# Kernel tuning notes

Measured on AMD Instinct MI355X. Metric: run time of the kernel, lower is better.

Reference implementation:

```python
import jax, jax.numpy as jnp
import numpy as np

HIDDEN = 1024
HEADS = 16
HEAD_DIM = HIDDEN // HEADS  # 64
B, S = 2, 2048


def setup_inputs() -> dict:
    key = jax.random.key(0)
    ks = jax.random.split(key, 12)
    lim_h = 1.0 / np.sqrt(HEAD_DIM)
    lim_o = 1.0 / np.sqrt(HIDDEN)
    u = lambda k, shape, lim: jax.random.uniform(k, shape, jnp.float32, -lim, lim)
    return {
        "query": jax.random.normal(ks[0], (B, S, HIDDEN), jnp.float32),
        "key": jax.random.normal(ks[1], (B, S, HIDDEN), jnp.float32),
        "value": jax.random.normal(ks[2], (B, S, HIDDEN), jnp.float32),
        "mask": jax.random.randint(ks[3], (B, 1, S, S), 0, 2, jnp.int32),
        "Wq": u(ks[4], (HEAD_DIM, HEAD_DIM), lim_h), "bq": u(ks[5], (HEAD_DIM,), lim_h),
        "Wk": u(ks[6], (HEAD_DIM, HEAD_DIM), lim_h), "bk": u(ks[7], (HEAD_DIM,), lim_h),
        "Wv": u(ks[8], (HEAD_DIM, HEAD_DIM), lim_h), "bv": u(ks[9], (HEAD_DIM,), lim_h),
        "Wo": u(ks[10], (HIDDEN, HIDDEN), lim_o), "bo": u(ks[11], (HIDDEN,), lim_o),
    }


def reference(query, key, value, mask, Wq, bq, Wk, bk, Wv, bv, Wo, bo):
    b = query.shape[0]
    # view [B, S, H, D]; per-head linear is SHARED across heads (head_dim x head_dim)
    q = query.reshape(b, -1, HEADS, HEAD_DIM) @ Wq.T + bq
    k = key.reshape(b, -1, HEADS, HEAD_DIM) @ Wk.T + bk
    v = value.reshape(b, -1, HEADS, HEAD_DIM) @ Wv.T + bv
    scores = jnp.einsum('nqhd,nkhd->nhqk', q, k)  # [B, H, Sq, Sk]
    scores = jnp.where(mask == 0, jnp.float32(-1e20), scores)
    # NOTE: original scales by sqrt(hidden_dim), not sqrt(head_dim)
    attn = jax.nn.softmax(scores / np.sqrt(HIDDEN).astype(np.float32), axis=3)
    out = jnp.einsum('nhql,nlhd->nqhd', attn, v).reshape(b, query.shape[1], HIDDEN)
    return out @ Wo.T + bo
```

## Files before the change

kernel.cpp:

```cpp
#include <hip/hip_runtime.h>
#include <hip/hip_bf16.h>

#define NB 2
#define NS 2048
#define NH 16
#define ND 64
#define NHID 1024

#define QSCALE 0.045084220f

typedef __attribute__((ext_vector_type(8))) short bf16x8;
typedef __attribute__((ext_vector_type(4))) short s16x4;
typedef __attribute__((ext_vector_type(4))) float f32x4;

typedef __attribute__((address_space(3))) unsigned int lds_u32;
typedef __attribute__((address_space(1))) unsigned int glb_u32;

__device__ inline void gl_lds16(const void* g, void* l) {
  __builtin_amdgcn_global_load_lds((const glb_u32*)g, (lds_u32*)l, 16, 0, 0);
}

__device__ inline short f2bf(float f) {
  __hip_bfloat16 h = __float2bfloat16(f);
  short s; __builtin_memcpy(&s, &h, 2); return s;
}

__device__ inline float selbit(float e, unsigned long long m) {
  float r;
  asm("v_cndmask_b32 %0, 0, %1, %2" : "=v"(r) : "v"(e), "s"(m));
  return r;
}

__device__ inline bf16x8 cvt8(const float* __restrict__ p) {
  float4 x = *(const float4*)p;
  float4 y = *(const float4*)(p + 4);
  bf16x8 r;
  r[0] = f2bf(x.x); r[1] = f2bf(x.y); r[2] = f2bf(x.z); r[3] = f2bf(x.w);
  r[4] = f2bf(y.x); r[5] = f2bf(y.y); r[6] = f2bf(y.z); r[7] = f2bf(y.w);
  return r;
}

__global__ __launch_bounds__(256) void prep(
    const int* __restrict__ mask, unsigned long long* __restrict__ mp,
    const float* __restrict__ Wq, const float* __restrict__ Wk,
    const float* __restrict__ Wv, const float* __restrict__ Wo,
    short* __restrict__ Wq_b, short* __restrict__ Wk_b,
    short* __restrict__ Wv_b, short* __restrict__ Wo_b)
{
  if (blockIdx.x < 512) {
    int tg = blockIdx.x * 256 + threadIdx.x;
    int q4 = tg & 3;
    int g4 = tg >> 2;
    int mt = g4 & 3, kt = (g4 >> 2) & 31, qg = (g4 >> 7) & 127, b = g4 >> 14;
    unsigned long long wq[4] = {0ull, 0ull, 0ull, 0ull};
#pragma unroll
    for (int cc = 0; cc < 4; ++cc) {
      int c2 = q4 * 4 + cc;
      const int4* p = (const int4*)(mask +
          ((size_t)(b * NS + qg * 16 + c2) * NS) + kt * 64 + mt * 16);
#pragma unroll
      for (int qq2 = 0; qq2 < 4; ++qq2) {
        int4 v = p[qq2];
        int sh = qq2 * 16 + c2;
        wq[0] |= (unsigned long long)(v.x != 0) << sh;
        wq[1] |= (unsigned long long)(v.y != 0) << sh;
        wq[2] |= (unsigned long long)(v.z != 0) << sh;
        wq[3] |= (unsigned long long)(v.w != 0) << sh;
      }
    }
#pragma unroll
    for (int r = 0; r < 4; ++r) {
      wq[r] |= __shfl_xor(wq[r], 1);
      wq[r] |= __shfl_xor(wq[r], 2);
    }
    mp[(size_t)g4 * 4 + q4] = wq[q4];
  } else {
    int i = ((blockIdx.x - 512) * 256 + threadIdx.x) * 4;
    const float* src; short* dst; int off; float sc = 1.0f;
    if (i < 1048576)      { src = Wo; dst = Wo_b; off = i; }
    else {
      int j = i - 1048576;
      if (j < 4096)       { src = Wq; dst = Wq_b; off = j; sc = QSCALE; }
      else if (j < 8192)  { src = Wk; dst = Wk_b; off = j - 4096; }
      else                { src = Wv; dst = Wv_b; off = j - 8192; }
    }
    float4 v = *(const float4*)(src + off);
    s16x4 o;
    o[0] = f2bf(v.x * sc); o[1] = f2bf(v.y * sc);
    o[2] = f2bf(v.z * sc); o[3] = f2bf(v.w * sc);
    *(s16x4*)(dst + off) = o;
  }
}

__global__ __launch_bounds__(256) void qk_proj(
    const float* __restrict__ qin, const float* __restrict__ kin,
    const short* __restrict__ Wq_b, const float* __restrict__ bq,
    const short* __restrict__ Wk_b, const float* __restrict__ bk,
    short* __restrict__ Qws, short* __restrict__ Kws)
{
  __shared__ __align__(16) short ldsT[4][16][72];
  const int tid = threadIdx.x;
  const int w = tid >> 6, lane = tid & 63;
  const int c = lane & 15, qq = lane >> 4;
  const int t = blockIdx.x * 4 + w;
  const int b = t >> 11, s = t & (NS - 1);
  const int aoff = (t * 16 + c) * 64 + qq * 8;
  const int row0 = lane >> 3, inner = lane & 7;

#pragma unroll
  for (int m = 0; m < 2; ++m) {
    const float* X  = (m == 0) ? qin  : kin;
    const short* W  = (m == 0) ? Wq_b : Wk_b;
    const float* bb = (m == 0) ? bq   : bk;
    short* dst      = (m == 0) ? Qws  : Kws;
    const float bsc = (m == 0) ? QSCALE : 1.0f;

    bf16x8 a0 = cvt8(X + aoff);
    bf16x8 a1 = cvt8(X + aoff + 32);

#pragma unroll
    for (int nt = 0; nt < 4; ++nt) {
      f32x4 z = {0.f, 0.f, 0.f, 0.f};
      const short* wp = W + (nt * 16 + c) * 64 + qq * 8;
      bf16x8 b0 = *(const bf16x8*)(wp);
      bf16x8 b1 = *(const bf16x8*)(wp + 32);
      z = __builtin_amdgcn_mfma_f32_16x16x32_bf16(a0, b0, z, 0, 0, 0);
      z = __builtin_amdgcn_mfma_f32_16x16x32_bf16(a1, b1, z, 0, 0, 0);
      float bias = bb[nt * 16 + c] * bsc;
#pragma unroll
      for (int r = 0; r < 4; ++r)
        ldsT[w][qq * 4 + r][nt * 16 + c] = f2bf(z[r] + bias);
    }

    bf16x8 v0 = *(const bf16x8*)&ldsT[w][row0][inner * 8];
    bf16x8 v1 = *(const bf16x8*)&ldsT[w][row0 + 8][inner * 8];
    int bh0 = b * NH + row0, bh1 = b * NH + row0 + 8;
    *(bf16x8*)(dst + (bh0 * NS + s) * 64 + inner * 8) = v0;
    *(bf16x8*)(dst + (bh1 * NS + s) * 64 + inner * 8) = v1;
  }
}

__global__ __launch_bounds__(256) void vproj(
    const float* __restrict__ vin, const short* __restrict__ Wv_b,
    const float* __restrict__ bv, short* __restrict__ Vt)
{
  __shared__ __align__(16) short ldsVT[64][72];
  const int tid = threadIdx.x;
  const int g = tid >> 6, lane = tid & 63;
  const int c = lane & 15, qq = lane >> 4;
  const int bh = blockIdx.x >> 5;
  const int stile = blockIdx.x & 31;
  const int b = bh >> 4, h = bh & 15;
  const int sb = stile * 64;

  bf16x8 wv[8];
  float bias[4];
#pragma unroll
  for (int nt = 0; nt < 4; ++nt) {
    const short* wp = Wv_b + (nt * 16 + c) * 64 + qq * 8;
    wv[nt * 2]     = *(const bf16x8*)(wp);
    wv[nt * 2 + 1] = *(const bf16x8*)(wp + 32);
    bias[nt] = bv[nt * 16 + c];
  }

  const float* ap = vin + ((size_t)((b * NS + sb + 16 * g + c) * 16 + h)) * 64 + qq * 8;
  bf16x8 a0 = cvt8(ap);
  bf16x8 a1 = cvt8(ap + 32);
#pragma unroll
  for (int nt = 0; nt < 4; ++nt) {
    f32x4 z = {0.f, 0.f, 0.f, 0.f};
    z = __builtin_amdgcn_mfma_f32_16x16x32_bf16(a0, wv[nt * 2], z, 0, 0, 0);
    z = __builtin_amdgcn_mfma_f32_16x16x32_bf16(a1, wv[nt * 2 + 1], z, 0, 0, 0);
    ushort4 u;
    u.x = (unsigned short)f2bf(z[0] + bias[nt]);
    u.y = (unsigned short)f2bf(z[1] + bias[nt]);
    u.z = (unsigned short)f2bf(z[2] + bias[nt]);
    u.w = (unsigned short)f2bf(z[3] + bias[nt]);
    *(ushort4*)&ldsVT[nt * 16 + c][16 * g + qq * 4] = u;
  }
  __syncthreads();

#pragma unroll
  for (int j = 0; j < 2; ++j) {
    int idx = tid + 256 * j;
    int d = idx >> 3, unit = idx & 7;
    bf16x8 o = *(const bf16x8*)&ldsVT[d][unit * 8];
    *(bf16x8*)(Vt + ((size_t)(bh * 64 + d)) * NS + sb + unit * 8) = o;
  }
}

__global__ __launch_bounds__(256, 4) void attn(
    const short* __restrict__ Qws, const short* __restrict__ Kws,
    const short* __restrict__ Vt, const unsigned long long* __restrict__ Mp,
    short* __restrict__ AO)
{
  __shared__ __align__(16) short Ks[2][64][64];
  __shared__ __align__(16) short Vs[2][64][64];
  __shared__ __align__(16) short Ps[4][16][64];

  const int tid = threadIdx.x;
  const int w = tid >> 6, lane = tid & 63;
  const int c = lane & 15, qq = lane >> 4;
  const int bh = blockIdx.x & 31;
  const int qtile = blockIdx.x >> 5;
  const int b = bh >> 4, h = bh & 15;
  const int qbase = qtile * 64 + w * 16;
  const int ca2 = (lane & 7) << 1;

  const short* Qp = Qws + (size_t)bh * (NS * 64);
  const short* Kp = Kws + (size_t)bh * (NS * 64);
  const short* Vp = Vt + (size_t)bh * (64 * NS);

  const int wu = __builtin_amdgcn_readfirstlane(w);
  const unsigned long long* mbase =
      Mp + (size_t)(b * (NS / 16) + qtile * 4 + wu) * ((NS / 64) * 16);

  bf16x8 aq0, aq1;
  {
    const short* qp = Qp + (qbase + c) * 64 + qq * 8;
    aq0 = *(const bf16x8*)(qp);
    aq1 = *(const bf16x8*)(qp + 32);
  }

  float lsum = 0.f;
  f32x4 O[4];
#pragma unroll
  for (int dt = 0; dt < 4; ++dt) { f32x4 z = {0.f, 0.f, 0.f, 0.f}; O[dt] = z; }

  short* Pw = &Ps[w][c][0];

  const int srow = lane >> 3;
  const int sunit = (lane & 7) ^ srow;
  auto stage = [&](int kt, int buf) {
#pragma unroll
    for (int i = 0; i < 2; ++i) {
      int j = w * 2 + i;
      const short* gk = Kp + ((size_t)(kt * 64 + j * 8 + srow)) * 64 + sunit * 8;
      gl_lds16(gk, &Ks[buf][0][0] + j * 512);
      const short* gv = Vp + ((size_t)(j * 8 + srow)) * NS + kt * 64 + sunit * 8;
      gl_lds16(gv, &Vs[buf][0][0] + j * 512);
    }
  };

  stage(0, 0);
  __syncthreads();

  for (int kt = 0; kt < NS / 64; ++kt) {
    const int buf = kt & 1;
    if (kt < NS / 64 - 1) stage(kt + 1, buf ^ 1);

    unsigned long long mw[16];
#pragma unroll
    for (int i = 0; i < 16; ++i) mw[i] = mbase[(size_t)kt * 16 + i];

    f32x4 st[4];
#pragma unroll
    for (int mt = 0; mt < 4; ++mt) {
      const short* kb = &Ks[buf][mt * 16 + c][0];
      bf16x8 ak0 = *(const bf16x8*)(kb + ((qq ^ (c & 7)) << 3));
      bf16x8 ak1 = *(const bf16x8*)(kb + (((4 + qq) ^ (c & 7)) << 3));
      f32x4 z = {0.f, 0.f, 0.f, 0.f};
      z = __builtin_amdgcn_mfma_f32_16x16x32_bf16(ak0, aq0, z, 0, 0, 0);
      z = __builtin_amdgcn_mfma_f32_16x16x32_bf16(ak1, aq1, z, 0, 0, 0);
      st[mt] = z;
    }

#pragma unroll
    for (int mt = 0; mt < 4; ++mt) {
      f32x4 s = st[mt];
      float e0 = selbit(__builtin_amdgcn_exp2f(s[0]), mw[mt * 4 + 0]);
      float e1 = selbit(__builtin_amdgcn_exp2f(s[1]), mw[mt * 4 + 1]);
      float e2 = selbit(__builtin_amdgcn_exp2f(s[2]), mw[mt * 4 + 2]);
      float e3 = selbit(__builtin_amdgcn_exp2f(s[3]), mw[mt * 4 + 3]);
      lsum += (e0 + e1) + (e2 + e3);
      ushort4 u;
      u.x = (unsigned short)f2bf(e0);
      u.y = (unsigned short)f2bf(e1);
      u.z = (unsigned short)f2bf(e2);
      u.w = (unsigned short)f2bf(e3);
      *(ushort4*)&Pw[((mt * 4 + qq) ^ ca2) << 2] = u;
    }

#pragma unroll
    for (int ks = 0; ks < 2; ++ks) {
      bf16x8 pf = *(const bf16x8*)&Pw[((ks * 8 + qq * 2) ^ ca2) << 2];
#pragma unroll
      for (int dt = 0; dt < 4; ++dt) {
        const short* vb = &Vs[buf][dt * 16 + c][0];
        bf16x8 vf = *(const bf16x8*)(vb + ((((ks << 2) + qq) ^ (c & 7)) << 3));
        O[dt] = __builtin_amdgcn_mfma_f32_16x16x32_bf16(vf, pf, O[dt], 0, 0, 0);
      }
    }

    __syncthreads();
  }

  {
    float v = lsum;
    v += __shfl_xor(v, 16);
    v += __shfl_xor(v, 32);
    lsum = 1.0f / fmaxf(v, 1e-30f);
  }

  const int row = qbase + c;
#pragma unroll
  for (int dt = 0; dt < 4; ++dt) {
    ushort4 u;
    u.x = (unsigned short)f2bf(O[dt][0] * lsum);
    u.y = (unsigned short)f2bf(O[dt][1] * lsum);
    u.z = (unsigned short)f2bf(O[dt][2] * lsum);
    u.w = (unsigned short)f2bf(O[dt][3] * lsum);
    *(ushort4*)(AO + ((size_t)(b * NS + row)) * NHID + h * 64 + dt * 16 + qq * 4) = u;
  }
}

__global__ __launch_bounds__(256, 2) void oproj(
    const short* __restrict__ X, const short* __restrict__ Wo_b,
    const float* __restrict__ bo, float* __restrict__ out)
{
  __shared__ __align__(16) short As[2][64][64];
  __shared__ __align__(16) short Bs[2][128][64];
  const int tid = threadIdx.x;
  const int w = tid >> 6, lane = tid & 63;
  const int c = lane & 15, qq = lane >> 4;
  const int rowbase = blockIdx.x * 64;
  const int colbase = blockIdx.y * 128;
  const int mh = w & 1, nh = w >> 1;

  const int srow = lane >> 3;
  const int sunit = (lane & 7) ^ srow;

  auto stage = [&](int kb, int buf) {
#pragma unroll
    for (int i = 0; i < 6; ++i) {
      int t = w * 6 + i;
      if (t < 8) {
        const short* g = X + (size_t)(rowbase + t * 8 + srow) * NHID
                           + kb * 64 + sunit * 8;
        gl_lds16(g, &As[buf][0][0] + t * 512);
      } else {
        int j = t - 8;
        const short* g = Wo_b + (size_t)(colbase + j * 8 + srow) * NHID
                              + kb * 64 + sunit * 8;
        gl_lds16(g, &Bs[buf][0][0] + j * 512);
      }
    }
  };

  f32x4 acc[2][4];
#pragma unroll
  for (int mt = 0; mt < 2; ++mt)
#pragma unroll
    for (int nt = 0; nt < 4; ++nt) { f32x4 z = {0.f, 0.f, 0.f, 0.f}; acc[mt][nt] = z; }

  stage(0, 0);
  __syncthreads();

  for (int kb = 0; kb < NHID / 64; ++kb) {
    const int buf = kb & 1;
    if (kb < NHID / 64 - 1) stage(kb + 1, buf ^ 1);

    bf16x8 af[2][2];
#pragma unroll
    for (int mt = 0; mt < 2; ++mt) {
      const short* ap = &As[buf][mh * 32 + mt * 16 + c][0];
#pragma unroll
      for (int ks = 0; ks < 2; ++ks)
        af[mt][ks] = *(const bf16x8*)(ap + ((((ks << 2) + qq) ^ (c & 7)) << 3));
    }
#pragma unroll
    for (int nt = 0; nt < 4; ++nt) {
      const short* bp = &Bs[buf][nh * 64 + nt * 16 + c][0];
#pragma unroll
      for (int ks = 0; ks < 2; ++ks) {
        bf16x8 bf = *(const bf16x8*)(bp + ((((ks << 2) + qq) ^ (c & 7)) << 3));
#pragma unroll
        for (int mt = 0; mt < 2; ++mt)
          acc[mt][nt] = __builtin_amdgcn_mfma_f32_16x16x32_bf16(af[mt][ks], bf, acc[mt][nt], 0, 0, 0);
      }
    }

    __syncthreads();
  }

#pragma unroll
  for (int nt = 0; nt < 4; ++nt) {
    int col = colbase + nh * 64 + nt * 16 + c;
    float bias = bo[col];
#pragma unroll
    for (int mt = 0; mt < 2; ++mt) {
      int row = rowbase + mh * 32 + mt * 16 + qq * 4;
#pragma unroll
      for (int r = 0; r < 4; ++r)
        out[(size_t)(row + r) * NHID + col] = acc[mt][nt][r] + bias;
    }
  }
}

extern "C" void kernel_launch(void* const* d_in, const int* in_sizes, int n_in,
                              void* d_out, int out_size, void* d_ws, size_t ws_size,
                              hipStream_t stream) {
  const float* qin = (const float*)d_in[0];
  const float* kin = (const float*)d_in[1];
  const float* vin = (const float*)d_in[2];
  const int*  mask = (const int*)d_in[3];
  const float* Wq = (const float*)d_in[4];
  const float* bq = (const float*)d_in[5];
  const float* Wk = (const float*)d_in[6];
  const float* bk = (const float*)d_in[7];
  const float* Wv = (const float*)d_in[8];
  const float* bv = (const float*)d_in[9];
  const float* Wo = (const float*)d_in[10];
  const float* bo = (const float*)d_in[11];
  float* out = (float*)d_out;

  char* ws = (char*)d_ws;
  short* Qws = (short*)(ws);
  short* Kws = (short*)(ws + (size_t)(8 << 20));
  short* Vt  = (short*)(ws + (size_t)(16 << 20));
  short* AO  = (short*)(ws + (size_t)(24 << 20));
  unsigned long long* Mp = (unsigned long long*)(ws + (size_t)(32 << 20));
  short* Wo_b = (short*)(ws + (size_t)(33 << 20));
  short* Wq_b = (short*)(ws + (size_t)(35 << 20));
  short* Wk_b = (short*)(ws + (size_t)(35 << 20) + 8192);
  short* Wv_b = (short*)(ws + (size_t)(35 << 20) + 16384);

  prep<<<1548, 256, 0, stream>>>(mask, Mp, Wq, Wk, Wv, Wo, Wq_b, Wk_b, Wv_b, Wo_b);
  qk_proj<<<NB * NS / 4, 256, 0, stream>>>(qin, kin, Wq_b, bq, Wk_b, bk, Qws, Kws);
  vproj<<<(NB * NH) * (NS / 64), 256, 0, stream>>>(vin, Wv_b, bv, Vt);
  attn<<<(NB * NH) * (NS / 64), 256, 0, stream>>>(Qws, Kws, Vt, Mp, AO);
  oproj<<<dim3(64, 8), 256, 0, stream>>>(AO, Wo_b, bo, out);
}
```

Before: 212.5 us.

## Load K/V fragments directly from global memory in attention and coalesce mask packing

The attention kernel no longer stages K and V tiles through double-buffered shared memory with async global-to-LDS loads and per-iteration barriers. Each wave now loads its MFMA fragments straight from global memory into registers. This removes LDS traffic and the block-wide sync, but every wave in a block now fetches the same K/V data on its own, which relies on L2/L1 hits and exposes global latency without explicit prefetching. Separately, the mask bit-packing in prep remaps threads so the four partial words are combined across lanes 16 and 32 apart instead of neighbouring lanes, changing its memory access pattern.

```diff
diff --git a/kernel.cpp b/kernel.cpp
--- a/kernel.cpp
+++ b/kernel.cpp
@@ -48,9 +48,10 @@
     short* __restrict__ Wv_b, short* __restrict__ Wo_b)
 {
   if (blockIdx.x < 512) {
-    int tg = blockIdx.x * 256 + threadIdx.x;
-    int q4 = tg & 3;
-    int g4 = tg >> 2;
+    int idx = blockIdx.x * 256 + threadIdx.x;
+    int lane = threadIdx.x & 63;
+    int q4 = lane >> 4;
+    int g4 = ((idx >> 6) << 4) | (lane & 15);
     int mt = g4 & 3, kt = (g4 >> 2) & 31, qg = (g4 >> 7) & 127, b = g4 >> 14;
     unsigned long long wq[4] = {0ull, 0ull, 0ull, 0ull};
 #pragma unroll
@@ -70,8 +71,8 @@
     }
 #pragma unroll
     for (int r = 0; r < 4; ++r) {
-      wq[r] |= __shfl_xor(wq[r], 1);
-      wq[r] |= __shfl_xor(wq[r], 2);
+      wq[r] |= __shfl_xor(wq[r], 16);
+      wq[r] |= __shfl_xor(wq[r], 32);
     }
     mp[(size_t)g4 * 4 + q4] = wq[q4];
   } else {
@@ -194,8 +195,6 @@
     const short* __restrict__ Vt, const unsigned long long* __restrict__ Mp,
     short* __restrict__ AO)
 {
-  __shared__ __align__(16) short Ks[2][64][64];
-  __shared__ __align__(16) short Vs[2][64][64];
   __shared__ __align__(16) short Ps[4][16][64];
 
   const int tid = threadIdx.x;
@@ -228,26 +227,23 @@
   for (int dt = 0; dt < 4; ++dt) { f32x4 z = {0.f, 0.f, 0.f, 0.f}; O[dt] = z; }
 
   short* Pw = &Ps[w][c][0];
-
-  const int srow = lane >> 3;
-  const int sunit = (lane & 7) ^ srow;
-  auto stage = [&](int kt, int buf) {
-#pragma unroll
-    for (int i = 0; i < 2; ++i) {
-      int j = w * 2 + i;
-      const short* gk = Kp + ((size_t)(kt * 64 + j * 8 + srow)) * 64 + sunit * 8;
-      gl_lds16(gk, &Ks[buf][0][0] + j * 512);
-      const short* gv = Vp + ((size_t)(j * 8 + srow)) * NS + kt * 64 + sunit * 8;
-      gl_lds16(gv, &Vs[buf][0][0] + j * 512);
-    }
-  };
-
-  stage(0, 0);
-  __syncthreads();
+  const short* kfb = Kp + c * 64 + qq * 8;
+  const short* vfb = Vp + (size_t)c * NS + qq * 8;
 
   for (int kt = 0; kt < NS / 64; ++kt) {
-    const int buf = kt & 1;
-    if (kt < NS / 64 - 1) stage(kt + 1, buf ^ 1);
+    bf16x8 ak[4][2];
+#pragma unroll
+    for (int mt = 0; mt < 4; ++mt) {
+      const short* kp = kfb + (kt * 64 + mt * 16) * 64;
+      ak[mt][0] = *(const bf16x8*)(kp);
+      ak[mt][1] = *(const bf16x8*)(kp + 32);
+    }
+    bf16x8 vf[2][4];
+#pragma unroll
+    for (int ks = 0; ks < 2; ++ks)
+#pragma unroll
+      for (int dt = 0; dt < 4; ++dt)
+        vf[ks][dt] = *(const bf16x8*)(vfb + (size_t)(dt * 16) * NS + kt * 64 + ks * 32);
 
     unsigned long long mw[16];
 #pragma unroll
@@ -256,12 +252,9 @@
     f32x4 st[4];
 #pragma unroll
     for (int mt = 0; mt < 4; ++mt) {
-      const short* kb = &Ks[buf][mt * 16 + c][0];
-      bf16x8 ak0 = *(const bf16x8*)(kb + ((qq ^ (c & 7)) << 3));
-      bf16x8 ak1 = *(const bf16x8*)(kb + (((4 + qq) ^ (c & 7)) << 3));
       f32x4 z = {0.f, 0.f, 0.f, 0.f};
-      z = __builtin_amdgcn_mfma_f32_16x16x32_bf16(ak0, aq0, z, 0, 0, 0);
-      z = __builtin_amdgcn_mfma_f32_16x16x32_bf16(ak1, aq1, z, 0, 0, 0);
+      z = __builtin_amdgcn_mfma_f32_16x16x32_bf16(ak[mt][0], aq0, z, 0, 0, 0);
+      z = __builtin_amdgcn_mfma_f32_16x16x32_bf16(ak[mt][1], aq1, z, 0, 0, 0);
       st[mt] = z;
     }
 
@@ -285,14 +278,9 @@
     for (int ks = 0; ks < 2; ++ks) {
       bf16x8 pf = *(const bf16x8*)&Pw[((ks * 8 + qq * 2) ^ ca2) << 2];
 #pragma unroll
-      for (int dt = 0; dt < 4; ++dt) {
-        const short* vb = &Vs[buf][dt * 16 + c][0];
-        bf16x8 vf = *(const bf16x8*)(vb + ((((ks << 2) + qq) ^ (c & 7)) << 3));
-        O[dt] = __builtin_amdgcn_mfma_f32_16x16x32_bf16(vf, pf, O[dt], 0, 0, 0);
-      }
-    }
-
-    __syncthreads();
+      for (int dt = 0; dt < 4; ++dt)
+        O[dt] = __builtin_amdgcn_mfma_f32_16x16x32_bf16(vf[ks][dt], pf, O[dt], 0, 0, 0);
+    }
   }
 
   {
```

After: 384.9 us. 81.1% more time.
